# Performance work log

Measured on AMD Instinct MI355X. Metric: run time of the kernel, lower is better.

The kernel has to match this reference:

```python
import jax, jax.numpy as jnp
import numpy as np

HEADS = 48
HEAD_DIM = 64
DIM = 3072
RANK = 128
TEXT_LEN = 226
VID_LEN = 1822
B = 1
LORA_W = 1.0
EPS = 1e-5


def setup_inputs() -> dict:
    key = jax.random.key(0)
    ks = jax.random.split(key, 24)
    s = 0.02  # weight init scale
    inp = {
        "hidden_states": jax.random.normal(ks[0], (B, VID_LEN, DIM), jnp.float32),
        "encoder_hidden_states": jax.random.normal(ks[1], (B, TEXT_LEN, DIM), jnp.float32),
        "rope_cos": jax.random.uniform(ks[2], (VID_LEN, HEAD_DIM), jnp.float32),
        "rope_sin": jax.random.uniform(ks[3], (VID_LEN, HEAD_DIM), jnp.float32),
        "Wq": jax.random.normal(ks[4], (DIM, DIM), jnp.float32) * s,
        "bq": jax.random.normal(ks[5], (DIM,), jnp.float32) * s,
        "Wk": jax.random.normal(ks[6], (DIM, DIM), jnp.float32) * s,
        "bk": jax.random.normal(ks[7], (DIM,), jnp.float32) * s,
        "Wv": jax.random.normal(ks[8], (DIM, DIM), jnp.float32) * s,
        "bv": jax.random.normal(ks[9], (DIM,), jnp.float32) * s,
        "Wo": jax.random.normal(ks[10], (DIM, DIM), jnp.float32) * s,
        "bo": jax.random.normal(ks[11], (DIM,), jnp.float32) * s,
        "lq_down": jax.random.normal(ks[12], (RANK, DIM), jnp.float32) / RANK,
        "lq_up": jax.random.normal(ks[13], (DIM, RANK), jnp.float32) * s,
        "lk_down": jax.random.normal(ks[14], (RANK, DIM), jnp.float32) / RANK,
        "lk_up": jax.random.normal(ks[15], (DIM, RANK), jnp.float32) * s,
        "lv_down": jax.random.normal(ks[16], (RANK, DIM), jnp.float32) / RANK,
        "lv_up": jax.random.normal(ks[17], (DIM, RANK), jnp.float32) * s,
        "lp_down": jax.random.normal(ks[18], (RANK, DIM), jnp.float32) / RANK,
        "lp_up": jax.random.normal(ks[19], (DIM, RANK), jnp.float32) * s,
        "gamma_q": jnp.ones((HEAD_DIM,), jnp.float32),
        "beta_q": jnp.zeros((HEAD_DIM,), jnp.float32),
        "gamma_k": jnp.ones((HEAD_DIM,), jnp.float32),
        "beta_k": jnp.zeros((HEAD_DIM,), jnp.float32),
    }
    return inp


def _lora(x, down, up):
    # x: [B,S,DIM]; down: [RANK,DIM]; up: [DIM,RANK]
    return (x @ down.T) @ up.T


def _layernorm(x, gamma, beta):
    mu = jnp.mean(x, axis=-1, keepdims=True)
    var = jnp.mean(jnp.square(x - mu), axis=-1, keepdims=True)
    return (x - mu) * jax.lax.rsqrt(var + EPS) * gamma + beta


def _apply_rope(x, cos, sin):
    # diffusers apply_rotary_emb, use_real=True, unbind_dim=-1
    # x: [B,H,S,D]; cos/sin: [S,D]
    xr = x.reshape(*x.shape[:-1], HEAD_DIM // 2, 2)
    x1, x2 = xr[..., 0], xr[..., 1]
    x_rot = jnp.stack([-x2, x1], axis=-1).reshape(x.shape)
    return x * cos + x_rot * sin


def reference(hidden_states, encoder_hidden_states, rope_cos, rope_sin,
              Wq, bq, Wk, bk, Wv, bv, Wo, bo,
              lq_down, lq_up, lk_down, lk_up, lv_down, lv_up, lp_down, lp_up,
              gamma_q, beta_q, gamma_k, beta_k):
    h = jnp.concatenate([encoder_hidden_states, hidden_states], axis=1)  # [B,S,DIM]
    S = h.shape[1]

    q = h @ Wq.T + bq + _lora(h, lq_down, lq_up) * LORA_W
    k = h @ Wk.T + bk + _lora(h, lk_down, lk_up) * LORA_W
    v = h @ Wv.T + bv + _lora(h, lv_down, lv_up) * LORA_W

    def split_heads(x):  # [B,S,DIM] -> [B,H,S,D]
        return x.reshape(B, S, HEADS, HEAD_DIM).transpose(0, 2, 1, 3)

    q, k, v = split_heads(q), split_heads(k), split_heads(v)
    q = _layernorm(q, gamma_q, beta_q)
    k = _layernorm(k, gamma_k, beta_k)

    # RoPE on video tokens only
    q = q.at[:, :, TEXT_LEN:].set(_apply_rope(q[:, :, TEXT_LEN:], rope_cos, rope_sin))
    k = k.at[:, :, TEXT_LEN:].set(_apply_rope(k[:, :, TEXT_LEN:], rope_cos, rope_sin))

    # scaled dot-product attention (no mask, no dropout)
    scale = 1.0 / np.sqrt(HEAD_DIM).astype(np.float32)
    scores = jnp.einsum("bhqd,bhkd->bhqk", q, k) * scale
    probs = jax.nn.softmax(scores, axis=-1)
    attn_out = jnp.einsum("bhqk,bhkd->bhqd", probs, v)

    out = attn_out.transpose(0, 2, 1, 3).reshape(B, S, DIM)
    out = out @ Wo.T + bo + _lora(out, lp_down, lp_up) * LORA_W

    enc_out = out[:, :TEXT_LEN, :]
    hid_out = out[:, TEXT_LEN:, :]
    return (hid_out, enc_out)
```

## Files before the change

### kernel.cpp

```cpp
#include <hip/hip_runtime.h>
#include <hip/hip_bf16.h>
#include <stdint.h>

#define S_TOT 2048
#define TEXT 226
#define VID 1822
#define DIM 3072
#define NH 48
#define HD 64

typedef __bf16 bf16x8 __attribute__((ext_vector_type(8)));
typedef __bf16 bf16x4 __attribute__((ext_vector_type(4)));
typedef float f32x4 __attribute__((ext_vector_type(4)));

#define AS1 __attribute__((address_space(1)))
#define AS3 __attribute__((address_space(3)))

__device__ __forceinline__ void g2l16(const void* g, void* l) {
    __builtin_amdgcn_global_load_lds((const AS1 uint32_t*)(uintptr_t)g,
                                     (AS3 uint32_t*)(uintptr_t)l, 16, 0, 0);
}

__device__ __forceinline__ f32x4 mfma16(bf16x4 a, bf16x4 b, f32x4 c) {
#if __has_builtin(__builtin_amdgcn_mfma_f32_16x16x16bf16_1k)
    typedef short s4 __attribute__((ext_vector_type(4)));
    union U { bf16x4 b; s4 s; };
    U ua, ub; ua.b = a; ub.b = b;
    return __builtin_amdgcn_mfma_f32_16x16x16bf16_1k(ua.s, ub.s, c, 0, 0, 0);
#else
    f32x4 d = c;
    asm volatile("v_mfma_f32_16x16x16_bf16 %0, %1, %2, %0"
                 : "+v"(d) : "v"(a), "v"(b));
    return d;
#endif
}

#define ARENA_N 47431680ull

struct NormArgs { const void* p[24]; };

__global__ __launch_bounds__(256)
void normalize_inputs(NormArgs a, __bf16* __restrict__ arena)
{
    static constexpr unsigned long long segStart[25] = {
        0ull, 694272ull, 6291456ull, 15728640ull, 25165824ull, 34603008ull,
        44040192ull, 44433408ull, 44826624ull, 45219840ull, 45613056ull,
        46006272ull, 46399488ull, 46792704ull, 47185920ull, 47302528ull,
        47419136ull, 47422208ull, 47425280ull, 47428352ull, 47431424ull,
        47431488ull, 47431552ull, 47431616ull, 47431680ull };
    static constexpr int segIn[24] = {
        1, 0, 4, 6, 8, 10, 12, 13, 14, 15, 16, 17, 18, 19, 2, 3,
        5, 7, 9, 11, 20, 21, 22, 23 };

    const uint32_t w0 = *(const uint32_t*)a.p[20];
    const bool f32in = (w0 == 0x3F800000u);

    const size_t i0 = ((size_t)blockIdx.x * 256 + threadIdx.x) * 8;
    if (i0 >= ARENA_N) return;
    int s = 0;
    while (i0 >= segStart[s + 1]) s++;
    const size_t off = i0 - segStart[s];

    if (f32in) {
        const float* src = (const float*)a.p[segIn[s]] + off;
        const float4 v0 = ((const float4*)src)[0];
        const float4 v1 = ((const float4*)src)[1];
        bf16x8 o;
        o[0] = (__bf16)v0.x; o[1] = (__bf16)v0.y; o[2] = (__bf16)v0.z; o[3] = (__bf16)v0.w;
        o[4] = (__bf16)v1.x; o[5] = (__bf16)v1.y; o[6] = (__bf16)v1.z; o[7] = (__bf16)v1.w;
        *(bf16x8*)(arena + i0) = o;
    } else {
        const __bf16* src = (const __bf16*)a.p[segIn[s]] + off;
        *(uint4*)(arena + i0) = *(const uint4*)src;
    }
}

__device__ __forceinline__ void mm_chunks(
    const __bf16* __restrict__ Ag, int lda, const __bf16* __restrict__ Bg, int ldb,
    int kbeg, int kend, f32x4 (&acc)[4][4], __bf16* As, __bf16* Bs,
    int wave, int srow, int l15, int quad, int wm, int wn)
{
    for (int k0 = kbeg; k0 < kend; k0 += 32) {
        __syncthreads();
#pragma unroll
        for (int i = 0; i < 2; i++) {
            const int blk = i * 4 + wave;
            const int r = blk * 16 + srow;
            g2l16(Ag + (size_t)r * lda + k0, &As[blk * 512]);
            g2l16(Bg + (size_t)r * ldb + k0, &Bs[blk * 512]);
        }
        __syncthreads();
        bf16x8 af[4], bfr[4];
#pragma unroll
        for (int i = 0; i < 4; i++)
            af[i] = *(const bf16x8*)&As[(wm + i * 16 + l15) * 32 + quad * 8];
#pragma unroll
        for (int j = 0; j < 4; j++)
            bfr[j] = *(const bf16x8*)&Bs[(wn + j * 16 + l15) * 32 + quad * 8];
#pragma unroll
        for (int i = 0; i < 4; i++)
#pragma unroll
            for (int j = 0; j < 4; j++)
                acc[i][j] = __builtin_amdgcn_mfma_f32_16x16x32_bf16(af[i], bfr[j], acc[i][j], 0, 0, 0);
    }
}

template<bool ATOMIC, bool FUSE2, bool TO_OUT>
__global__ __launch_bounds__(256)
void gemm_bt(const __bf16* __restrict__ A, int lda,
             const __bf16* __restrict__ B0, const __bf16* __restrict__ B1,
             const __bf16* __restrict__ B2, int ldb,
             const __bf16* __restrict__ bias0, const __bf16* __restrict__ bias1,
             const __bf16* __restrict__ bias2,
             const __bf16* __restrict__ A2, int lda2, int a2ColOff,
             const __bf16* __restrict__ U0, const __bf16* __restrict__ U1,
             const __bf16* __restrict__ U2, int ldu,
             float* __restrict__ C, int ldc,
             int K, int K2, int tilesPerGroup, int kChunk,
             void* __restrict__ dout, const void* __restrict__ probe)
{
    __shared__ __bf16 As[128 * 32];
    __shared__ __bf16 Bs[128 * 32];
    const int tid  = threadIdx.x;
    const int wave = tid >> 6;
    const int lane = tid & 63;
    const int l15  = lane & 15, quad = lane >> 4;
    const int bm = blockIdx.x, bn = blockIdx.y;
    const int group = bn / tilesPerGroup;
    const int nt    = bn - group * tilesPerGroup;
    const __bf16* B    = (group == 0) ? B0 : ((group == 1) ? B1 : B2);
    const __bf16* bias = (group == 0) ? bias0 : ((group == 1) ? bias1 : bias2);

    const int k0s = blockIdx.z * kChunk;
    int k0e = k0s + kChunk; if (k0e > K) k0e = K;

    const int srow = lane >> 2;
    const int schk = (lane & 3) * 8;
    const __bf16* Ag = A + (size_t)(bm * 128) * lda + schk;
    const __bf16* Bg = B + (size_t)(nt * 128) * ldb + schk;

    f32x4 acc[4][4] = {};
    const int wm = (wave & 1) * 64;
    const int wn = (wave >> 1) * 64;

    mm_chunks(Ag, lda, Bg, ldb, k0s, k0e, acc, As, Bs, wave, srow, l15, quad, wm, wn);

    if (FUSE2) {
        const __bf16* U = (group == 0) ? U0 : ((group == 1) ? U1 : U2);
        const __bf16* A2g = A2 + group * a2ColOff + (size_t)(bm * 128) * lda2 + schk;
        const __bf16* Ug  = U + (size_t)(nt * 128) * ldu + schk;
        mm_chunks(A2g, lda2, Ug, ldu, 0, K2, acc, As, Bs, wave, srow, l15, quad, wm, wn);
    }

    bool f32out = false;
    if (TO_OUT) f32out = (*(const uint32_t*)probe == 0x3F800000u);

#pragma unroll
    for (int i = 0; i < 4; i++) {
#pragma unroll
        for (int j = 0; j < 4; j++) {
            const int coll = wn + j * 16 + l15;
            const int col  = bn * 128 + coll;
            float bv = 0.f;
            if (bias) bv = (float)bias[nt * 128 + coll];
#pragma unroll
            for (int r = 0; r < 4; r++) {
                const int row = bm * 128 + wm + i * 16 + quad * 4 + r;
                float v = acc[i][j][r] + bv;
                if (TO_OUT) {
                    const size_t mrow = (row < TEXT) ? (size_t)(row + VID) : (size_t)(row - TEXT);
                    if (f32out) ((float*)dout)[mrow * DIM + col] = v;
                    else        ((__bf16*)dout)[mrow * DIM + col] = (__bf16)v;
                } else if (ATOMIC) {
                    atomicAdd(C + (size_t)row * ldc + col, v);
                } else {
                    C[(size_t)row * ldc + col] = v;
                }
            }
        }
    }
}

__global__ __launch_bounds__(256)
void ln_rope(const float* __restrict__ qkv,
             const __bf16* __restrict__ gq, const __bf16* __restrict__ bq,
             const __bf16* __restrict__ gk, const __bf16* __restrict__ bk,
             const __bf16* __restrict__ cosb, const __bf16* __restrict__ sinb,
             __bf16* __restrict__ qh, __bf16* __restrict__ kh)
{
    const int s = blockIdx.x;
    const int wave = threadIdx.x >> 6, lane = threadIdx.x & 63;
    for (int idx = wave; idx < 2 * NH; idx += 4) {
        const int mat  = idx / NH;
        const int head = idx - mat * NH;
        float x = qkv[(size_t)s * 9216 + mat * DIM + head * HD + lane];
        float mu = x;
        mu += __shfl_xor(mu, 1, 64);  mu += __shfl_xor(mu, 2, 64);
        mu += __shfl_xor(mu, 4, 64);  mu += __shfl_xor(mu, 8, 64);
        mu += __shfl_xor(mu, 16, 64); mu += __shfl_xor(mu, 32, 64);
        mu *= 0.015625f;
        float d = x - mu;
        float vv = d * d;
        vv += __shfl_xor(vv, 1, 64);  vv += __shfl_xor(vv, 2, 64);
        vv += __shfl_xor(vv, 4, 64);  vv += __shfl_xor(vv, 8, 64);
        vv += __shfl_xor(vv, 16, 64); vv += __shfl_xor(vv, 32, 64);
        vv *= 0.015625f;
        const float g = (float)(mat ? gk[lane] : gq[lane]);
        const float b = (float)(mat ? bk[lane] : bq[lane]);
        float y = d * rsqrtf(vv + 1e-5f) * g + b;
        if (s >= TEXT) {
            const int pos = s - TEXT;
            const float c  = (float)cosb[pos * HD + lane];
            const float sn = (float)sinb[pos * HD + lane];
            const float oth = __shfl_xor(y, 1, 64);
            const float rot = (lane & 1) ? oth : -oth;
            y = y * c + rot * sn;
        }
        __bf16* dst = mat ? kh : qh;
        dst[((size_t)head * S_TOT + s) * HD + lane] = (__bf16)y;
    }
}

__global__ __launch_bounds__(256)
void vtrans(const float* __restrict__ qkv, __bf16* __restrict__ vt)
{
    __shared__ float tile[64][65];
    const int h = blockIdx.x, sb = blockIdx.y;
    const int tid = threadIdx.x;
    const int r0 = tid >> 4;
    const int c0 = (tid & 15) * 4;
#pragma unroll
    for (int p = 0; p < 4; p++) {
        const int r = p * 16 + r0;
        const float4 v = *(const float4*)&qkv[((size_t)(sb * 64 + r)) * 9216 + 2 * DIM + h * HD + c0];
        tile[r][c0 + 0] = v.x; tile[r][c0 + 1] = v.y;
        tile[r][c0 + 2] = v.z; tile[r][c0 + 3] = v.w;
    }
    __syncthreads();
#pragma unroll
    for (int p = 0; p < 4; p++) {
        const int d = p * 16 + r0;
        __bf16 o[4];
#pragma unroll
        for (int e = 0; e < 4; e++) o[e] = (__bf16)tile[c0 + e][d];
        *(uint2*)&vt[((size_t)(h * HD + d)) * S_TOT + sb * 64 + c0] = *(const uint2*)o;
    }
}

#define KS_LD 72
#define VS_LD 136

__global__ __launch_bounds__(256)
void flash_attn(const __bf16* __restrict__ qh, const __bf16* __restrict__ kh,
                const __bf16* __restrict__ vt, __bf16* __restrict__ outp)
{
    __shared__ __bf16 Ks[128 * KS_LD];
    __shared__ __bf16 Vs[64 * VS_LD];
    const int qb = blockIdx.x, h = blockIdx.y;
    const int tid = threadIdx.x, wave = tid >> 6, lane = tid & 63;
    const int l15 = lane & 15, quad = lane >> 4;

    bf16x8 qf[2][2];
#pragma unroll
    for (int t = 0; t < 2; t++)
#pragma unroll
        for (int ks = 0; ks < 2; ks++) {
            const __bf16* p = qh + ((size_t)(h * S_TOT + qb * 128 + wave * 32 + t * 16 + l15)) * HD
                                 + ks * 32 + quad * 8;
            bf16x8 v = *(const bf16x8*)p;
#pragma unroll
            for (int e = 0; e < 8; e++) v[e] = (__bf16)((float)v[e] * 0.125f);
            qf[t][ks] = v;
        }

    f32x4 of[2][4] = {};
    float m_i[2] = {-1e30f, -1e30f};
    float l_i[2] = {0.f, 0.f};
    const float L2E = 1.44269504f;

    for (int kb = 0; kb < S_TOT / 128; kb++) {
        bf16x8 kr[4], vr[4];
#pragma unroll
        for (int p = 0; p < 4; p++) {
            const int id = p * 256 + tid;
            const int krow = id >> 3, kc = (id & 7) * 8;
            kr[p] = *(const bf16x8*)(kh + ((size_t)(h * S_TOT + kb * 128 + krow)) * HD + kc);
            const int vrow = id >> 4, vc = (id & 15) * 8;
            vr[p] = *(const bf16x8*)(vt + ((size_t)(h * HD + vrow)) * S_TOT + kb * 128 + vc);
        }
        __syncthreads();
#pragma unroll
        for (int p = 0; p < 4; p++) {
            const int id = p * 256 + tid;
            const int krow = id >> 3, kc = (id & 7) * 8;
            *(bf16x8*)&Ks[krow * KS_LD + kc] = kr[p];
            const int vrow = id >> 4, vc = (id & 15) * 8;
            *(bf16x8*)&Vs[vrow * VS_LD + vc] = vr[p];
        }
        __syncthreads();

        f32x4 sf[2][8];
#pragma unroll
        for (int n = 0; n < 8; n++) {
            const bf16x8 k0 = *(const bf16x8*)&Ks[(n * 16 + l15) * KS_LD + quad * 8];
            const bf16x8 k1 = *(const bf16x8*)&Ks[(n * 16 + l15) * KS_LD + 32 + quad * 8];
#pragma unroll
            for (int t = 0; t < 2; t++) {
                f32x4 z = {0.f, 0.f, 0.f, 0.f};
                z = __builtin_amdgcn_mfma_f32_16x16x32_bf16(k0, qf[t][0], z, 0, 0, 0);
                sf[t][n] = __builtin_amdgcn_mfma_f32_16x16x32_bf16(k1, qf[t][1], z, 0, 0, 0);
            }
        }

        float alpha_l[2];
#pragma unroll
        for (int t = 0; t < 2; t++) {
            float mx = sf[t][0][0];
#pragma unroll
            for (int n = 0; n < 8; n++)
#pragma unroll
                for (int r = 0; r < 4; r++) mx = fmaxf(mx, sf[t][n][r]);
            mx = fmaxf(mx, __shfl_xor(mx, 16, 64));
            mx = fmaxf(mx, __shfl_xor(mx, 32, 64));
            const float mnew = fmaxf(m_i[t], mx);
            alpha_l[t] = __builtin_amdgcn_exp2f((m_i[t] - mnew) * L2E);
            m_i[t] = mnew;
            float rs = 0.f;
#pragma unroll
            for (int n = 0; n < 8; n++)
#pragma unroll
                for (int r = 0; r < 4; r++) {
                    const float pv = __builtin_amdgcn_exp2f((sf[t][n][r] - mnew) * L2E);
                    sf[t][n][r] = pv;
                    rs += pv;
                }
            rs += __shfl_xor(rs, 16, 64);
            rs += __shfl_xor(rs, 32, 64);
            l_i[t] = l_i[t] * alpha_l[t] + rs;
        }

        bf16x4 pf[2][8];
#pragma unroll
        for (int t = 0; t < 2; t++)
#pragma unroll
            for (int kk = 0; kk < 8; kk++) {
                bf16x4 o;
                o[0] = (__bf16)sf[t][kk][0]; o[1] = (__bf16)sf[t][kk][1];
                o[2] = (__bf16)sf[t][kk][2]; o[3] = (__bf16)sf[t][kk][3];
                pf[t][kk] = o;
            }

#pragma unroll
        for (int t = 0; t < 2; t++)
#pragma unroll
            for (int r = 0; r < 4; r++) {
                const float a_r = __shfl(alpha_l[t], quad * 4 + r, 16);
#pragma unroll
                for (int j = 0; j < 4; j++) of[t][j][r] *= a_r;
            }

#pragma unroll
        for (int kk = 0; kk < 8; kk++) {
#pragma unroll
            for (int j = 0; j < 4; j++) {
                const bf16x4 vf = *(const bf16x4*)&Vs[(j * 16 + l15) * VS_LD + kk * 16 + quad * 4];
                of[0][j] = mfma16(pf[0][kk], vf, of[0][j]);
                of[1][j] = mfma16(pf[1][kk], vf, of[1][j]);
            }
        }
    }

#pragma unroll
    for (int t = 0; t < 2; t++)
#pragma unroll
        for (int r = 0; r < 4; r++) {
            const float lr = __shfl(l_i[t], quad * 4 + r, 16);
            const float inv = 1.f / lr;
            const int row = qb * 128 + wave * 32 + t * 16 + quad * 4 + r;
#pragma unroll
            for (int j = 0; j < 4; j++)
                outp[(size_t)row * DIM + h * HD + j * 16 + l15] = (__bf16)(of[t][j][r] * inv);
        }
}

__global__ __launch_bounds__(256)
void f32_to_bf16(const float* __restrict__ src, __bf16* __restrict__ dst, int n4)
{
    const int i = blockIdx.x * blockDim.x + threadIdx.x;
    if (i < n4) {
        const float4 v = ((const float4*)src)[i];
        __bf16 o[4] = {(__bf16)v.x, (__bf16)v.y, (__bf16)v.z, (__bf16)v.w};
        ((uint2*)dst)[i] = *(const uint2*)o;
    }
}

extern "C" void kernel_launch(void* const* d_in, const int* in_sizes, int n_in,
                              void* d_out, int out_size, void* d_ws, size_t ws_size,
                              hipStream_t stream)
{
    char* ws = (char*)d_ws;
    __bf16* arena = (__bf16*)ws;

    const __bf16* h     = arena + 0;
    const __bf16* Wq    = arena + 6291456;
    const __bf16* Wk    = arena + 15728640;
    const __bf16* Wv    = arena + 25165824;
    const __bf16* Wo    = arena + 34603008;
    const __bf16* lqd   = arena + 44040192;
    const __bf16* lqu   = arena + 44433408;
    const __bf16* lkd   = arena + 44826624;
    const __bf16* lku   = arena + 45219840;
    const __bf16* lvd   = arena + 45613056;
    const __bf16* lvu   = arena + 46006272;
    const __bf16* lpd   = arena + 46399488;
    const __bf16* lpu   = arena + 46792704;
    const __bf16* ropec = arena + 47185920;
    const __bf16* ropes = arena + 47302528;
    const __bf16* bq    = arena + 47419136;
    const __bf16* bk    = arena + 47422208;
    const __bf16* bv    = arena + 47425280;
    const __bf16* bo    = arena + 47428352;
    const __bf16* gq    = arena + 47431424;
    const __bf16* btq   = arena + 47431488;
    const __bf16* gk    = arena + 47431552;
    const __bf16* btk   = arena + 47431616;

    float*  qkvf = (float*)(ws + 94863360);
    float*  t32  = (float*)(ws + 170360832);
    __bf16* t16  = (__bf16*)(ws + 174555136);
    __bf16* qh   = (__bf16*)(ws + 176652288);
    __bf16* kh   = (__bf16*)(ws + 189235200);
    __bf16* vt   = (__bf16*)(ws + 201818112);
    __bf16* attn = (__bf16*)(ws + 0);

    NormArgs na;
    for (int i = 0; i < 24; i++) na.p[i] = d_in[i];
    normalize_inputs<<<(unsigned)((ARENA_N / 8 + 255) / 256), 256, 0, stream>>>(na, arena);

    hipMemsetAsync(t32, 0, (size_t)2048 * 512 * 4, stream);

    gemm_bt<true, false, false><<<dim3(16, 3, 4), 256, 0, stream>>>(
        h, DIM, lqd, lkd, lvd, DIM, nullptr, nullptr, nullptr,
        nullptr, 0, 0, nullptr, nullptr, nullptr, 0,
        t32, 512, DIM, 0, 1, 768, nullptr, nullptr);
    f32_to_bf16<<<(2048 * 512 / 4 + 255) / 256, 256, 0, stream>>>(t32, t16, 2048 * 512 / 4);

    gemm_bt<false, true, false><<<dim3(16, 72, 1), 256, 0, stream>>>(
        h, DIM, Wq, Wk, Wv, DIM, bq, bk, bv,
        t16, 512, 128, lqu, lku, lvu, 128,
        qkvf, 9216, DIM, 128, 24, DIM, nullptr, nullptr);

    ln_rope<<<2048, 256, 0, stream>>>(qkvf, gq, btq, gk, btk, ropec, ropes, qh, kh);
    vtrans<<<dim3(48, 32), 256, 0, stream>>>(qkvf, vt);
    flash_attn<<<dim3(16, 48), 256, 0, stream>>>(qh, kh, vt, attn);

    gemm_bt<true, false, false><<<dim3(16, 1, 4), 256, 0, stream>>>(
        attn, DIM, lpd, lpd, lpd, DIM, nullptr, nullptr, nullptr,
        nullptr, 0, 0, nullptr, nullptr, nullptr, 0,
        t32 + 384, 512, DIM, 0, 1, 768, nullptr, nullptr);
    f32_to_bf16<<<(2048 * 512 / 4 + 255) / 256, 256, 0, stream>>>(t32, t16, 2048 * 512 / 4);

    gemm_bt<false, true, true><<<dim3(16, 24, 1), 256, 0, stream>>>(
        attn, DIM, Wo, Wo, Wo, DIM, bo, bo, bo,
        t16 + 384, 512, 0, lpu, lpu, lpu, 128,
        nullptr, 0, DIM, 128, 24, DIM, d_out, d_in[20]);
}
```

Measured before the change: 716.3 us.

## Swizzle GEMM LDS, store QKV as bf16, prefetch flash-attn tiles, raise split-K

Several changes at once. GEMM LDS tiles get an XOR-style chunk swizzle on both the global-to-LDS writes and the fragment reads, aimed at reducing bank conflicts. The QKV projection now writes bf16 instead of fp32, halving intermediate traffic for ln_rope and vtrans at some precision cost. Flash attention register-prefetches the next K/V block while computing the current one and restructures the softmax loop to reduce register pressure. The LoRA down-projection split-K factors are doubled or quadrupled for more parallelism, at the cost of more atomics.

```diff
diff --git a/kernel.cpp b/kernel.cpp
--- a/kernel.cpp
+++ b/kernel.cpp
@@ -78,7 +78,7 @@
 __device__ __forceinline__ void mm_chunks(
     const __bf16* __restrict__ Ag, int lda, const __bf16* __restrict__ Bg, int ldb,
     int kbeg, int kend, f32x4 (&acc)[4][4], __bf16* As, __bf16* Bs,
-    int wave, int srow, int l15, int quad, int wm, int wn)
+    int wave, int srow, int schk, int rdoff, int l15, int wm, int wn)
 {
     for (int k0 = kbeg; k0 < kend; k0 += 32) {
         __syncthreads();
@@ -86,17 +86,17 @@
         for (int i = 0; i < 2; i++) {
             const int blk = i * 4 + wave;
             const int r = blk * 16 + srow;
-            g2l16(Ag + (size_t)r * lda + k0, &As[blk * 512]);
-            g2l16(Bg + (size_t)r * ldb + k0, &Bs[blk * 512]);
+            g2l16(Ag + (size_t)r * lda + k0 + schk, &As[blk * 512]);
+            g2l16(Bg + (size_t)r * ldb + k0 + schk, &Bs[blk * 512]);
         }
         __syncthreads();
         bf16x8 af[4], bfr[4];
 #pragma unroll
         for (int i = 0; i < 4; i++)
-            af[i] = *(const bf16x8*)&As[(wm + i * 16 + l15) * 32 + quad * 8];
+            af[i] = *(const bf16x8*)&As[(wm + i * 16 + l15) * 32 + rdoff];
 #pragma unroll
         for (int j = 0; j < 4; j++)
-            bfr[j] = *(const bf16x8*)&Bs[(wn + j * 16 + l15) * 32 + quad * 8];
+            bfr[j] = *(const bf16x8*)&Bs[(wn + j * 16 + l15) * 32 + rdoff];
 #pragma unroll
         for (int i = 0; i < 4; i++)
 #pragma unroll
@@ -105,7 +105,7 @@
     }
 }
 
-template<bool ATOMIC, bool FUSE2, bool TO_OUT>
+template<int MODE, bool ATOMIC, bool FUSE2>
 __global__ __launch_bounds__(256)
 void gemm_bt(const __bf16* __restrict__ A, int lda,
              const __bf16* __restrict__ B0, const __bf16* __restrict__ B1,
@@ -115,7 +115,7 @@
              const __bf16* __restrict__ A2, int lda2, int a2ColOff,
              const __bf16* __restrict__ U0, const __bf16* __restrict__ U1,
              const __bf16* __restrict__ U2, int ldu,
-             float* __restrict__ C, int ldc,
+             float* __restrict__ C, __bf16* __restrict__ Cb, int ldc,
              int K, int K2, int tilesPerGroup, int kChunk,
              void* __restrict__ dout, const void* __restrict__ probe)
 {
@@ -134,26 +134,27 @@
     const int k0s = blockIdx.z * kChunk;
     int k0e = k0s + kChunk; if (k0e > K) k0e = K;
 
-    const int srow = lane >> 2;
-    const int schk = (lane & 3) * 8;
-    const __bf16* Ag = A + (size_t)(bm * 128) * lda + schk;
-    const __bf16* Bg = B + (size_t)(nt * 128) * ldb + schk;
+    const int srow  = lane >> 2;
+    const int schk  = ((((lane & 3) - (lane >> 3)) & 3)) * 8;
+    const int rdoff = ((quad + (l15 >> 1)) & 3) * 8;
+    const __bf16* Ag = A + (size_t)(bm * 128) * lda;
+    const __bf16* Bg = B + (size_t)(nt * 128) * ldb;
 
     f32x4 acc[4][4] = {};
     const int wm = (wave & 1) * 64;
     const int wn = (wave >> 1) * 64;
 
-    mm_chunks(Ag, lda, Bg, ldb, k0s, k0e, acc, As, Bs, wave, srow, l15, quad, wm, wn);
+    mm_chunks(Ag, lda, Bg, ldb, k0s, k0e, acc, As, Bs, wave, srow, schk, rdoff, l15, wm, wn);
 
     if (FUSE2) {
         const __bf16* U = (group == 0) ? U0 : ((group == 1) ? U1 : U2);
-        const __bf16* A2g = A2 + group * a2ColOff + (size_t)(bm * 128) * lda2 + schk;
-        const __bf16* Ug  = U + (size_t)(nt * 128) * ldu + schk;
-        mm_chunks(A2g, lda2, Ug, ldu, 0, K2, acc, As, Bs, wave, srow, l15, quad, wm, wn);
+        const __bf16* A2g = A2 + group * a2ColOff + (size_t)(bm * 128) * lda2;
+        const __bf16* Ug  = U + (size_t)(nt * 128) * ldu;
+        mm_chunks(A2g, lda2, Ug, ldu, 0, K2, acc, As, Bs, wave, srow, schk, rdoff, l15, wm, wn);
     }
 
     bool f32out = false;
-    if (TO_OUT) f32out = (*(const uint32_t*)probe == 0x3F800000u);
+    if (MODE == 1) f32out = (*(const uint32_t*)probe == 0x3F800000u);
 
 #pragma unroll
     for (int i = 0; i < 4; i++) {
@@ -167,10 +168,12 @@
             for (int r = 0; r < 4; r++) {
                 const int row = bm * 128 + wm + i * 16 + quad * 4 + r;
                 float v = acc[i][j][r] + bv;
-                if (TO_OUT) {
+                if (MODE == 1) {
                     const size_t mrow = (row < TEXT) ? (size_t)(row + VID) : (size_t)(row - TEXT);
                     if (f32out) ((float*)dout)[mrow * DIM + col] = v;
                     else        ((__bf16*)dout)[mrow * DIM + col] = (__bf16)v;
+                } else if (MODE == 3) {
+                    Cb[(size_t)row * ldc + col] = (__bf16)v;
                 } else if (ATOMIC) {
                     atomicAdd(C + (size_t)row * ldc + col, v);
                 } else {
@@ -182,7 +185,7 @@
 }
 
 __global__ __launch_bounds__(256)
-void ln_rope(const float* __restrict__ qkv,
+void ln_rope(const __bf16* __restrict__ qkv,
              const __bf16* __restrict__ gq, const __bf16* __restrict__ bq,
              const __bf16* __restrict__ gk, const __bf16* __restrict__ bk,
              const __bf16* __restrict__ cosb, const __bf16* __restrict__ sinb,
@@ -193,7 +196,7 @@
     for (int idx = wave; idx < 2 * NH; idx += 4) {
         const int mat  = idx / NH;
         const int head = idx - mat * NH;
-        float x = qkv[(size_t)s * 9216 + mat * DIM + head * HD + lane];
+        float x = (float)qkv[(size_t)s * 9216 + mat * DIM + head * HD + lane];
         float mu = x;
         mu += __shfl_xor(mu, 1, 64);  mu += __shfl_xor(mu, 2, 64);
         mu += __shfl_xor(mu, 4, 64);  mu += __shfl_xor(mu, 8, 64);
@@ -222,7 +225,7 @@
 }
 
 __global__ __launch_bounds__(256)
-void vtrans(const float* __restrict__ qkv, __bf16* __restrict__ vt)
+void vtrans(const __bf16* __restrict__ qkv, __bf16* __restrict__ vt)
 {
     __shared__ float tile[64][65];
     const int h = blockIdx.x, sb = blockIdx.y;
@@ -232,9 +235,10 @@
 #pragma unroll
     for (int p = 0; p < 4; p++) {
         const int r = p * 16 + r0;
-        const float4 v = *(const float4*)&qkv[((size_t)(sb * 64 + r)) * 9216 + 2 * DIM + h * HD + c0];
-        tile[r][c0 + 0] = v.x; tile[r][c0 + 1] = v.y;
-        tile[r][c0 + 2] = v.z; tile[r][c0 + 3] = v.w;
+        const uint2 raw = *(const uint2*)&qkv[((size_t)(sb * 64 + r)) * 9216 + 2 * DIM + h * HD + c0];
+        const __bf16* b = (const __bf16*)&raw;
+#pragma unroll
+        for (int e = 0; e < 4; e++) tile[r][c0 + e] = (float)b[e];
     }
     __syncthreads();
 #pragma unroll
@@ -249,6 +253,22 @@
 
 #define KS_LD 72
 #define VS_LD 136
+#define NKB (S_TOT / 128)
+
+__device__ __forceinline__ void fa_load(const __bf16* __restrict__ kh,
+                                        const __bf16* __restrict__ vt,
+                                        int h, int kb, int tid,
+                                        bf16x8 (&kr)[4], bf16x8 (&vr)[4])
+{
+#pragma unroll
+    for (int p = 0; p < 4; p++) {
+        const int id = p * 256 + tid;
+        const int krow = id >> 3, kc = (id & 7) * 8;
+        kr[p] = *(const bf16x8*)(kh + ((size_t)(h * S_TOT + kb * 128 + krow)) * HD + kc);
+        const int vrow = id >> 4, vc = (id & 15) * 8;
+        vr[p] = *(const bf16x8*)(vt + ((size_t)(h * HD + vrow)) * S_TOT + kb * 128 + vc);
+    }
+}
 
 __global__ __launch_bounds__(256)
 void flash_attn(const __bf16* __restrict__ qh, const __bf16* __restrict__ kh,
@@ -278,16 +298,10 @@
     float l_i[2] = {0.f, 0.f};
     const float L2E = 1.44269504f;
 
-    for (int kb = 0; kb < S_TOT / 128; kb++) {
-        bf16x8 kr[4], vr[4];
-#pragma unroll
-        for (int p = 0; p < 4; p++) {
-            const int id = p * 256 + tid;
-            const int krow = id >> 3, kc = (id & 7) * 8;
-            kr[p] = *(const bf16x8*)(kh + ((size_t)(h * S_TOT + kb * 128 + krow)) * HD + kc);
-            const int vrow = id >> 4, vc = (id & 15) * 8;
-            vr[p] = *(const bf16x8*)(vt + ((size_t)(h * HD + vrow)) * S_TOT + kb * 128 + vc);
-        }
+    bf16x8 kr[4], vr[4];
+    fa_load(kh, vt, h, 0, tid, kr, vr);
+
+    for (int kb = 0; kb < NKB; kb++) {
         __syncthreads();
 #pragma unroll
         for (int p = 0; p < 4; p++) {
@@ -298,28 +312,26 @@
             *(bf16x8*)&Vs[vrow * VS_LD + vc] = vr[p];
         }
         __syncthreads();
-
-        f32x4 sf[2][8];
-#pragma unroll
-        for (int n = 0; n < 8; n++) {
-            const bf16x8 k0 = *(const bf16x8*)&Ks[(n * 16 + l15) * KS_LD + quad * 8];
-            const bf16x8 k1 = *(const bf16x8*)&Ks[(n * 16 + l15) * KS_LD + 32 + quad * 8];
-#pragma unroll
-            for (int t = 0; t < 2; t++) {
+        if (kb + 1 < NKB) fa_load(kh, vt, h, kb + 1, tid, kr, vr);
+
+        bf16x4 pf[2][8];
+        float alpha_l[2];
+#pragma unroll
+        for (int t = 0; t < 2; t++) {
+            f32x4 sf[8];
+#pragma unroll
+            for (int n = 0; n < 8; n++) {
+                const bf16x8 k0 = *(const bf16x8*)&Ks[(n * 16 + l15) * KS_LD + quad * 8];
+                const bf16x8 k1 = *(const bf16x8*)&Ks[(n * 16 + l15) * KS_LD + 32 + quad * 8];
                 f32x4 z = {0.f, 0.f, 0.f, 0.f};
                 z = __builtin_amdgcn_mfma_f32_16x16x32_bf16(k0, qf[t][0], z, 0, 0, 0);
-                sf[t][n] = __builtin_amdgcn_mfma_f32_16x16x32_bf16(k1, qf[t][1], z, 0, 0, 0);
+                sf[n] = __builtin_amdgcn_mfma_f32_16x16x32_bf16(k1, qf[t][1], z, 0, 0, 0);
             }
-        }
-
-        float alpha_l[2];
-#pragma unroll
-        for (int t = 0; t < 2; t++) {
-            float mx = sf[t][0][0];
+            float mx = sf[0][0];
 #pragma unroll
             for (int n = 0; n < 8; n++)
 #pragma unroll
-                for (int r = 0; r < 4; r++) mx = fmaxf(mx, sf[t][n][r]);
+                for (int r = 0; r < 4; r++) mx = fmaxf(mx, sf[n][r]);
             mx = fmaxf(mx, __shfl_xor(mx, 16, 64));
             mx = fmaxf(mx, __shfl_xor(mx, 32, 64));
             const float mnew = fmaxf(m_i[t], mx);
@@ -330,25 +342,21 @@
             for (int n = 0; n < 8; n++)
 #pragma unroll
                 for (int r = 0; r < 4; r++) {
-                    const float pv = __builtin_amdgcn_exp2f((sf[t][n][r] - mnew) * L2E);
-                    sf[t][n][r] = pv;
+                    const float pv = __builtin_amdgcn_exp2f((sf[n][r] - mnew) * L2E);
+                    sf[n][r] = pv;
                     rs += pv;
                 }
             rs += __shfl_xor(rs, 16, 64);
             rs += __shfl_xor(rs, 32, 64);
             l_i[t] = l_i[t] * alpha_l[t] + rs;
-        }
-
-        bf16x4 pf[2][8];
-#pragma unroll
-        for (int t = 0; t < 2; t++)
 #pragma unroll
             for (int kk = 0; kk < 8; kk++) {
                 bf16x4 o;
-                o[0] = (__bf16)sf[t][kk][0]; o[1] = (__bf16)sf[t][kk][1];
-                o[2] = (__bf16)sf[t][kk][2]; o[3] = (__bf16)sf[t][kk][3];
+                o[0] = (__bf16)sf[kk][0]; o[1] = (__bf16)sf[kk][1];
+                o[2] = (__bf16)sf[kk][2]; o[3] = (__bf16)sf[kk][3];
                 pf[t][kk] = o;
             }
+        }
 
 #pragma unroll
         for (int t = 0; t < 2; t++)
@@ -425,12 +433,12 @@
     const __bf16* gk    = arena + 47431552;
     const __bf16* btk   = arena + 47431616;
 
-    float*  qkvf = (float*)(ws + 94863360);
-    float*  t32  = (float*)(ws + 170360832);
-    __bf16* t16  = (__bf16*)(ws + 174555136);
-    __bf16* qh   = (__bf16*)(ws + 176652288);
-    __bf16* kh   = (__bf16*)(ws + 189235200);
-    __bf16* vt   = (__bf16*)(ws + 201818112);
+    __bf16* qkvb = (__bf16*)(ws + 94863360);
+    float*  t32  = (float*)(ws + 132612096);
+    __bf16* t16  = (__bf16*)(ws + 136806400);
+    __bf16* qh   = (__bf16*)(ws + 138903552);
+    __bf16* kh   = (__bf16*)(ws + 151486464);
+    __bf16* vt   = (__bf16*)(ws + 164069376);
     __bf16* attn = (__bf16*)(ws + 0);
 
     NormArgs na;
@@ -439,29 +447,29 @@
 
     hipMemsetAsync(t32, 0, (size_t)2048 * 512 * 4, stream);
 
-    gemm_bt<true, false, false><<<dim3(16, 3, 4), 256, 0, stream>>>(
+    gemm_bt<0, true, false><<<dim3(16, 3, 8), 256, 0, stream>>>(
         h, DIM, lqd, lkd, lvd, DIM, nullptr, nullptr, nullptr,
         nullptr, 0, 0, nullptr, nullptr, nullptr, 0,
-        t32, 512, DIM, 0, 1, 768, nullptr, nullptr);
+        t32, nullptr, 512, DIM, 0, 1, 384, nullptr, nullptr);
     f32_to_bf16<<<(2048 * 512 / 4 + 255) / 256, 256, 0, stream>>>(t32, t16, 2048 * 512 / 4);
 
-    gemm_bt<false, true, false><<<dim3(16, 72, 1), 256, 0, stream>>>(
+    gemm_bt<3, false, true><<<dim3(16, 72, 1), 256, 0, stream>>>(
         h, DIM, Wq, Wk, Wv, DIM, bq, bk, bv,
         t16, 512, 128, lqu, lku, lvu, 128,
-        qkvf, 9216, DIM, 128, 24, DIM, nullptr, nullptr);
-
-    ln_rope<<<2048, 256, 0, stream>>>(qkvf, gq, btq, gk, btk, ropec, ropes, qh, kh);
-    vtrans<<<dim3(48, 32), 256, 0, stream>>>(qkvf, vt);
+        nullptr, qkvb, 9216, DIM, 128, 24, DIM, nullptr, nullptr);
+
+    ln_rope<<<2048, 256, 0, stream>>>(qkvb, gq, btq, gk, btk, ropec, ropes, qh, kh);
+    vtrans<<<dim3(48, 32), 256, 0, stream>>>(qkvb, vt);
     flash_attn<<<dim3(16, 48), 256, 0, stream>>>(qh, kh, vt, attn);
 
-    gemm_bt<true, false, false><<<dim3(16, 1, 4), 256, 0, stream>>>(
+    gemm_bt<0, true, false><<<dim3(16, 1, 16), 256, 0, stream>>>(
         attn, DIM, lpd, lpd, lpd, DIM, nullptr, nullptr, nullptr,
         nullptr, 0, 0, nullptr, nullptr, nullptr, 0,
-        t32 + 384, 512, DIM, 0, 1, 768, nullptr, nullptr);
+        t32 + 384, nullptr, 512, DIM, 0, 1, 192, nullptr, nullptr);
     f32_to_bf16<<<(2048 * 512 / 4 + 255) / 256, 256, 0, stream>>>(t32, t16, 2048 * 512 / 4);
 
-    gemm_bt<false, true, true><<<dim3(16, 24, 1), 256, 0, stream>>>(
+    gemm_bt<1, false, true><<<dim3(16, 24, 1), 256, 0, stream>>>(
         attn, DIM, Wo, Wo, Wo, DIM, bo, bo, bo,
         t16 + 384, 512, 0, lpu, lpu, lpu, 128,
-        nullptr, 0, DIM, 128, 24, DIM, d_out, d_in[20]);
-}
+        nullptr, nullptr, DIM, DIM, 128, 24, DIM, d_out, d_in[20]);
+}
```

Measured after the change: 719.9 us. Within noise of the previous version (+0.5%).
